# Optimization experiments

Measured on AMD Instinct MI355X. Metric: run time of the kernel, lower is better.

## Reference

```python
import jax, jax.numpy as jnp
import numpy as np

B, S, Z = 64, 512, 256
HID, L = 1024, 1024


def _lstm_cell(x, h, c, Wih, Whh, bih, bhh):
    # torch LSTMCell gate order: i, f, g, o
    gates = x @ Wih.T + bih + h @ Whh.T + bhh  # [B, 4L]
    i, f, g, o = jnp.split(gates, 4, axis=-1)
    i, f, o = jax.nn.sigmoid(i), jax.nn.sigmoid(f), jax.nn.sigmoid(o)
    g = jnp.tanh(g)
    c_new = f * c + i * g
    h_new = o * jnp.tanh(c_new)
    return h_new, c_new


def setup_inputs() -> dict:
    key = jax.random.key(0)
    ks = jax.random.split(key, 16)
    sc = 0.05
    return {
        "z": jax.random.normal(ks[0], (B, S, Z), jnp.float32),
        "prev_gen0": jax.random.uniform(ks[1], (B, Z), jnp.float32),
        "h1": jnp.zeros((B, L), jnp.float32),
        "c1": jnp.zeros((B, L), jnp.float32),
        "h2": jnp.zeros((B, L), jnp.float32),
        "c2": jnp.zeros((B, L), jnp.float32),
        "W1": jax.random.normal(ks[2], (HID, 2 * Z), jnp.float32) * sc,
        "b1": jnp.zeros((HID,), jnp.float32),
        "Wih1": jax.random.normal(ks[3], (4 * L, HID), jnp.float32) * sc,
        "Whh1": jax.random.normal(ks[4], (4 * L, L), jnp.float32) * sc,
        "bih1": jnp.zeros((4 * L,), jnp.float32),
        "bhh1": jnp.zeros((4 * L,), jnp.float32),
        "Wih2": jax.random.normal(ks[5], (4 * L, L), jnp.float32) * sc,
        "Whh2": jax.random.normal(ks[6], (4 * L, L), jnp.float32) * sc,
        "bih2": jnp.zeros((4 * L,), jnp.float32),
        "bhh2": jnp.zeros((4 * L,), jnp.float32),
        "W2": jax.random.normal(ks[7], (Z, L), jnp.float32) * sc,
        "b2": jnp.zeros((Z,), jnp.float32),
    }


def reference(z, prev_gen0, h1, c1, h2, c2, W1, b1, Wih1, Whh1, bih1, bhh1,
              Wih2, Whh2, bih2, bhh2, W2, b2):
    z_t = jnp.transpose(z, (1, 0, 2))  # [S, B, Z]

    def step(carry, z_step):
        prev_gen, h1, c1, h2, c2 = carry
        concat_in = jnp.concatenate([z_step, prev_gen], axis=-1)  # [B, 2Z]
        out = jax.nn.relu(concat_in @ W1.T + b1)                  # [B, HID]
        h1, c1 = _lstm_cell(out, h1, c1, Wih1, Whh1, bih1, bhh1)
        # dropout disabled (inference / deterministic reference)
        h2, c2 = _lstm_cell(h1, h2, c2, Wih2, Whh2, bih2, bhh2)
        prev_gen = h2 @ W2.T + b2                                 # [B, Z]
        return (prev_gen, h1, c1, h2, c2), prev_gen

    (_, h1, c1, h2, c2), feats = jax.lax.scan(
        step, (prev_gen0, h1, c1, h2, c2), z_t)
    gen_feats = jnp.transpose(feats, (1, 0, 2))  # [B, S, Z]
    return gen_feats, (h1, c1), (h2, c2)
```

## Files before the change

### kernel.cpp

```cpp
#include <hip/hip_runtime.h>

#define NB 64
#define NS 512
#define NZ 256
#define NH 1024
#define NWG 256
#define NT 512

typedef _Float16 f16;
typedef unsigned long long u64;
typedef __attribute__((ext_vector_type(8))) _Float16 half8;
typedef __attribute__((ext_vector_type(4))) float f32x4;

#define WS_BAR  0
#define WS_B1P  32768
#define WS_PG0  36864
#define WS_WF   69632
#define WS_ACT  2166784
#define SLOTF 65536
#define REQ1 (2166784ull + 3ull * 513ull * 131072ull)

__device__ __forceinline__ float sigf(float x) { return 1.f / (1.f + __expf(-x)); }
__device__ __forceinline__ float tanhfast(float x) { return 2.f / (1.f + __expf(-2.f * x)) - 1.f; }

__device__ __forceinline__ f32x4 MF(half8 a, half8 b, f32x4 c) {
  return __builtin_amdgcn_mfma_f32_16x16x32_f16(a, b, c, 0, 0, 0);
}

__device__ __forceinline__ u64 ald8(const f16* p) {
  return __hip_atomic_load((const u64*)p, __ATOMIC_RELAXED, __HIP_MEMORY_SCOPE_AGENT);
}
template <bool CACHED>
__device__ __forceinline__ half8 ldc(const f16* base, int kk, int kg, int R) {
  int ch = 8 * kk + 2 * kg;
  union { u64 u[2]; half8 h; } x;
  if (CACHED) {
    x.u[0] = *(const u64*)(base + ((size_t)(ch * 64 + R) * 4));
    x.u[1] = *(const u64*)(base + ((size_t)((ch + 1) * 64 + R) * 4));
  } else {
    x.u[0] = ald8(base + ((size_t)(ch * 64 + R) * 4));
    x.u[1] = ald8(base + ((size_t)((ch + 1) * 64 + R) * 4));
  }
  return x.h;
}
__device__ __forceinline__ void ast4f(float* p, float v) {
  __hip_atomic_store((unsigned*)(void*)p, __float_as_uint(v), __ATOMIC_RELAXED, __HIP_MEMORY_SCOPE_AGENT);
}
__device__ __forceinline__ void store_act(f16* base, int w, int m, float hvf) {
  f16 hv = (f16)hvf;
  unsigned short hb; __builtin_memcpy(&hb, &hv, 2);
  int l = threadIdx.x & 63;
  int c_ = l & 15;
  int v1 = __shfl((int)hb, c_ + 16);
  int v2 = __shfl((int)hb, c_ + 32);
  int v3 = __shfl((int)hb, c_ + 48);
  if (l < 16) {
    int R = 16 * m + c_;
    u64 val = (u64)hb | ((u64)(unsigned short)v1 << 16)
            | ((u64)(unsigned short)v2 << 32) | ((u64)(unsigned short)v3 << 48);
    __hip_atomic_store((u64*)(base + ((size_t)(w * 64 + R) * 4)), val,
                       __ATOMIC_RELAXED, __HIP_MEMORY_SCOPE_AGENT);
  }
}
template <bool CACHED>
__device__ __forceinline__ void gemm_half(const f16* base, const char* brow, int bofs,
                                          int kh, int kg, int R, f32x4& a0, f32x4& a1) {
  #pragma unroll 8
  for (int i = 0; i < 16; ++i) {
    int kk = kh * 16 + i;
    half8 a = ldc<CACHED>(base, kk, kg, R);
    half8 b = *(const half8*)(brow + bofs + kk * 64);
    if (i & 1) a1 = MF(a, b, a1); else a0 = MF(a, b, a0);
  }
}

__device__ __forceinline__ void bar_arrive(char* bar, int w, unsigned e) {
  asm volatile("s_waitcnt vmcnt(0)" ::: "memory");
  __syncthreads();
  if (threadIdx.x == 0)
    __hip_atomic_store((unsigned*)(bar + (size_t)w * 128), e,
                       __ATOMIC_RELAXED, __HIP_MEMORY_SCOPE_AGENT);
}
__device__ __forceinline__ void bar_wait(char* bar, unsigned e) {
  if (threadIdx.x < 64) {
    const unsigned* c0 = (const unsigned*)(bar + (size_t)threadIdx.x * 128);
    for (;;) {
      unsigned v0 = __hip_atomic_load(c0,            __ATOMIC_RELAXED, __HIP_MEMORY_SCOPE_AGENT);
      unsigned v1 = __hip_atomic_load(c0 + 64 * 32,  __ATOMIC_RELAXED, __HIP_MEMORY_SCOPE_AGENT);
      unsigned v2 = __hip_atomic_load(c0 + 128 * 32, __ATOMIC_RELAXED, __HIP_MEMORY_SCOPE_AGENT);
      unsigned v3 = __hip_atomic_load(c0 + 192 * 32, __ATOMIC_RELAXED, __HIP_MEMORY_SCOPE_AGENT);
      int ok = (v0 >= e) & (v1 >= e) & (v2 >= e) & (v3 >= e);
      if (__all(ok)) break;
      __builtin_amdgcn_s_sleep(1);
    }
    asm volatile("" ::: "memory");
  }
  __syncthreads();
}

#define L_W0   0
#define L_W2   10304
#define L_W1   12368
#define L_WP2  78160
#define L_W1P  143952
#define L_X    146064
#define L_X2   150160
#define L_X3   154256
#define LDS_BYTES 154512

__global__ void init_state(const float* __restrict__ h1, const float* __restrict__ h2,
                           const float* __restrict__ pg0, const float* __restrict__ W1,
                           const float* __restrict__ b1, const float* __restrict__ b2,
                           char* __restrict__ ws, size_t h2off) {
  int i = blockIdx.x * blockDim.x + threadIdx.x;
  int R = i & 63;
  int U = i >> 6;
  f16* H1s0 = (f16*)(ws + WS_ACT);
  f16* H2s0 = (f16*)(ws + WS_ACT) + h2off;
  int pidx = ((U >> 2) * 64 + R) * 4 + (U & 3);
  H1s0[pidx] = (f16)h1[(size_t)R * NH + U];
  H2s0[pidx] = (f16)h2[(size_t)R * NH + U];
  if (i < 16384) {
    int u = i >> 6, r2 = i & 63;
    ((f16*)(ws + WS_PG0))[((u >> 2) * 64 + r2) * 4 + (u & 3)] = (f16)pg0[(size_t)r2 * NZ + u];
  }
  if (i < NH) {
    float acc = b1[i];
    const float* wp = W1 + (size_t)i * (2 * NZ) + NZ;
    for (int mm = 0; mm < NZ; ++mm) acc = fmaf(wp[mm], b2[mm], acc);
    ((float*)(ws + WS_B1P))[i] = acc;
  }
  if (i < 8192) ((unsigned*)(ws + WS_BAR))[i] = 0u;
}

__global__ void prep_wfused(const float* __restrict__ W1, const float* __restrict__ W2,
                            char* __restrict__ ws) {
  int u = blockIdx.x >> 2;
  int j = ((blockIdx.x & 3) << 8) + threadIdx.x;
  const float* wp = W1 + (size_t)u * (2 * NZ) + NZ;
  float acc = 0.f;
  for (int mm = 0; mm < NZ; ++mm) acc = fmaf(wp[mm], W2[(size_t)mm * NH + j], acc);
  ((f16*)(ws + WS_WF))[(size_t)u * NH + j] = (f16)acc;
}

template <bool CACHED>
__global__ __launch_bounds__(NT, 1) void gen_persistent(
    const float* __restrict__ z,
    const float* __restrict__ W1, const float* __restrict__ b1,
    const float* __restrict__ Wih1, const float* __restrict__ Whh1,
    const float* __restrict__ bih1, const float* __restrict__ bhh1,
    const float* __restrict__ Wih2, const float* __restrict__ Whh2,
    const float* __restrict__ bih2, const float* __restrict__ bhh2,
    const float* __restrict__ W2, const float* __restrict__ b2,
    const float* __restrict__ c1in, const float* __restrict__ c2in,
    float* __restrict__ dout, char* __restrict__ ws, size_t h2off, size_t outoff)
{
  extern __shared__ char smem[];
  const int w = blockIdx.x;
  const int tid = threadIdx.x;
  const int w8 = tid >> 6;
  const int m = w8 & 3;
  const int kh = w8 >> 2;
  const int l = tid & 63;
  const int c = l & 15;
  const int kg = l >> 4;

  f16* H1base = (f16*)(ws + WS_ACT);
  f16* H2base = H1base + h2off;
  f16* Outbase = H1base + outoff;
  const f16* Pg0p = (const f16*)(ws + WS_PG0);
  const f16* Wf = (const f16*)(ws + WS_WF);
  const float* b1p = (const float*)(ws + WS_B1P);
  char* bar = ws + WS_BAR;

  for (int i = 0; i < 16; ++i) {
    int gi = i >> 2, uu = 4 * w + (i & 3);
    const float* s1i = Wih1 + (size_t)(gi * NH + uu) * NH;
    const float* s1h = Whh1 + (size_t)(gi * NH + uu) * NH;
    const float* s2i = Wih2 + (size_t)(gi * NH + uu) * NH;
    const float* s2h = Whh2 + (size_t)(gi * NH + uu) * NH;
    f16* d1 = (f16*)(smem + L_W1 + i * 4112);
    f16* d2 = (f16*)(smem + L_WP2 + i * 4112);
    for (int k = tid; k < NH; k += NT) {
      d1[k] = (f16)s1i[k]; d1[NH + k] = (f16)s1h[k];
      d2[k] = (f16)s2i[k]; d2[NH + k] = (f16)s2h[k];
    }
  }
  for (int i = 0; i < 4; ++i) {
    int uu = 4 * w + i;
    f16* d0 = (f16*)(smem + L_W0 + i * 2576);
    if (tid < 256) d0[tid] = (f16)W1[(size_t)uu * (2 * NZ) + tid];
    for (int k = tid; k < NH; k += NT) d0[NZ + k] = Wf[(size_t)uu * NH + k];
    f16* dp = (f16*)(smem + L_W1P + i * 528);
    if (tid < 256) dp[tid] = (f16)W1[(size_t)uu * (2 * NZ) + NZ + tid];
  }
  {
    f16* dw2 = (f16*)(smem + L_W2);
    for (int k = tid; k < NH; k += NT) dw2[k] = (f16)W2[(size_t)w * NH + k];
  }
  __syncthreads();

  const int R = 16 * m + c;
  const int U = 4 * w + kg;
  const float b0fused = b1p[U];
  const float b0plain = b1[U];
  const float bi1 = bih1[U] + bhh1[U];
  const float bf1 = bih1[NH + U] + bhh1[NH + U];
  const float bg1 = bih1[2 * NH + U] + bhh1[2 * NH + U];
  const float bo1 = bih1[3 * NH + U] + bhh1[3 * NH + U];
  const float bi2 = bih2[U] + bhh2[U];
  const float bf2 = bih2[NH + U] + bhh2[NH + U];
  const float bg2 = bih2[2 * NH + U] + bhh2[2 * NH + U];
  const float bo2 = bih2[3 * NH + U] + bhh2[3 * NH + U];
  const float b2w = b2[w];

  float c1reg = c1in[(size_t)R * NH + U];
  float c2reg = c2in[(size_t)R * NH + U];
  float h1last = 0.f, h2last = 0.f;

  float* scr  = (float*)(smem + L_X) + m * 256;
  float* scr3 = (float*)(smem + L_X3) + m * 16;
  const char* brow0 = smem + L_W0 + (c & 3) * 2576 + kg * 16;
  const char* brow2 = smem + L_W2 + kg * 16;
  const char* brow1 = smem + L_W1 + c * 4112 + kg * 16;
  const char* browp2 = smem + L_WP2 + c * 4112 + kg * 16;
  const char* browp0 = smem + L_W1P + (c & 3) * 528 + kg * 16;
  const float* zlane = z + (size_t)R * NS * NZ + kg * 8;

  for (int t = 0; t < NS; ++t) {
    const int sp = CACHED ? t : (t & 1);
    const int sn = CACHED ? (t + 1) : ((t + 1) & 1);
    const f16* h2prev = H2base + (size_t)sp * SLOTF;
    const f16* h1prev = H1base + (size_t)sp * SLOTF;
    f16* h1new = H1base + (size_t)sn * SLOTF;
    f16* h2new = H2base + (size_t)sn * SLOTF;
    f16* outb = Outbase + (size_t)sn * SLOTF;
    const unsigned eb = 3u * (unsigned)t;

    f32x4 ao0 = {0.f,0.f,0.f,0.f}, ao1 = ao0, ap0 = ao0, ap1 = ao0;
    if (t == 0) {
      if (kh == 0) {
        #pragma unroll
        for (int kk = 0; kk < 8; ++kk) {
          f32x4 f0 = *(const f32x4*)(zlane + kk * 32);
          f32x4 f1 = *(const f32x4*)(zlane + kk * 32 + 4);
          half8 a;
          a[0]=(f16)f0[0]; a[1]=(f16)f0[1]; a[2]=(f16)f0[2]; a[3]=(f16)f0[3];
          a[4]=(f16)f1[0]; a[5]=(f16)f1[1]; a[6]=(f16)f1[2]; a[7]=(f16)f1[3];
          half8 b = *(const half8*)(brow0 + kk * 64);
          if (kk & 1) ao1 = MF(a, b, ao1); else ao0 = MF(a, b, ao0);
        }
      } else {
        #pragma unroll
        for (int kk = 0; kk < 8; ++kk) {
          half8 a = ldc<true>(Pg0p, kk, kg, R);
          half8 b = *(const half8*)(browp0 + kk * 64);
          if (kk & 1) ao1 = MF(a, b, ao1); else ao0 = MF(a, b, ao0);
        }
      }
      bar_wait(bar, eb);
    } else {
      const float* zt = zlane + (size_t)t * NZ;
      #pragma unroll
      for (int i = 0; i < 4; ++i) {
        int kk = kh * 4 + i;
        f32x4 f0 = *(const f32x4*)(zt + kk * 32);
        f32x4 f1 = *(const f32x4*)(zt + kk * 32 + 4);
        half8 a;
        a[0]=(f16)f0[0]; a[1]=(f16)f0[1]; a[2]=(f16)f0[2]; a[3]=(f16)f0[3];
        a[4]=(f16)f1[0]; a[5]=(f16)f1[1]; a[6]=(f16)f1[2]; a[7]=(f16)f1[3];
        half8 b = *(const half8*)(brow0 + kk * 64);
        if (i & 1) ao1 = MF(a, b, ao1); else ao0 = MF(a, b, ao0);
      }
      bar_wait(bar, eb);
      #pragma unroll 8
      for (int i = 0; i < 16; ++i) {
        int kk = kh * 16 + i;
        half8 a = ldc<CACHED>(h2prev, kk, kg, R);
        half8 bwf = *(const half8*)(brow0 + 512 + kk * 64);
        half8 bw2 = *(const half8*)(brow2 + kk * 64);
        if (i & 1) { ao1 = MF(a, bwf, ao1); ap1 = MF(a, bw2, ap1); }
        else       { ao0 = MF(a, bwf, ao0); ap0 = MF(a, bw2, ap0); }
      }
    }
    f32x4 Dp;
    {
      float* s2 = (float*)(smem + L_X2) + m * 256;
      f32x4 D = ao0 + ao1;
      Dp = ap0 + ap1;
      if (kh == 0) {
        if (c < 4) {
          #pragma unroll
          for (int v = 0; v < 4; ++v) s2[c * 16 + kg * 4 + v] = D[v];
        }
        if (c == 0 && t > 0) {
          #pragma unroll
          for (int v = 0; v < 4; ++v) scr3[kg * 4 + v] = Dp[v];
        }
      }
      __syncthreads();
      if (kh == 1) {
        if (c < 4) {
          #pragma unroll
          for (int v = 0; v < 4; ++v) scr[c * 16 + kg * 4 + v] = D[v] + s2[c * 16 + kg * 4 + v];
        }
        float pre = scr[kg * 16 + c] + ((t == 0) ? b0plain : b0fused);
        store_act(outb, w, m, fmaxf(pre, 0.f));
      }
    }
    bar_arrive(bar, w, eb + 1);
    if (kh == 1 && t > 0 && c == 0) {
      #pragma unroll
      for (int v = 0; v < 4; ++v) {
        int Rp = 16 * m + kg * 4 + v;
        ast4f(&dout[((size_t)Rp * NS + (t - 1)) * NZ + w], Dp[v] + scr3[kg * 4 + v] + b2w);
      }
    }

    {
      f32x4 g0 = {0.f,0.f,0.f,0.f}, g1 = g0;
      gemm_half<CACHED>(h1prev, brow1, 2048, kh, kg, R, g0, g1);
      bar_wait(bar, eb + 1);
      gemm_half<CACHED>(outb, brow1, 0, kh, kg, R, g0, g1);
      float* s2 = (float*)(smem + L_X2) + m * 256;
      f32x4 D = g0 + g1;
      if (kh == 0) {
        #pragma unroll
        for (int v = 0; v < 4; ++v) s2[c * 16 + kg * 4 + v] = D[v];
      }
      __syncthreads();
      if (kh == 1) {
        #pragma unroll
        for (int v = 0; v < 4; ++v) scr[c * 16 + kg * 4 + v] = D[v] + s2[c * 16 + kg * 4 + v];
        float ai = scr[kg * 16 + c];
        float af = scr[(4 + kg) * 16 + c];
        float ag = scr[(8 + kg) * 16 + c];
        float aoo = scr[(12 + kg) * 16 + c];
        float iv = sigf(ai + bi1), fv = sigf(af + bf1);
        float gv = tanhfast(ag + bg1), ov = sigf(aoo + bo1);
        float cn = fmaf(fv, c1reg, iv * gv);
        c1reg = cn;
        float hv = ov * tanhfast(cn);
        h1last = hv;
        store_act(h1new, w, m, hv);
      }
    }
    bar_arrive(bar, w, eb + 2);

    {
      f32x4 q0 = {0.f,0.f,0.f,0.f}, q1 = q0;
      gemm_half<CACHED>(h2prev, browp2, 2048, kh, kg, R, q0, q1);
      bar_wait(bar, eb + 2);
      gemm_half<CACHED>(h1new, browp2, 0, kh, kg, R, q0, q1);
      float* s2 = (float*)(smem + L_X2) + m * 256;
      f32x4 D = q0 + q1;
      if (kh == 0) {
        #pragma unroll
        for (int v = 0; v < 4; ++v) s2[c * 16 + kg * 4 + v] = D[v];
      }
      __syncthreads();
      if (kh == 1) {
        #pragma unroll
        for (int v = 0; v < 4; ++v) scr[c * 16 + kg * 4 + v] = D[v] + s2[c * 16 + kg * 4 + v];
        float ai = scr[kg * 16 + c];
        float af = scr[(4 + kg) * 16 + c];
        float ag = scr[(8 + kg) * 16 + c];
        float aoo = scr[(12 + kg) * 16 + c];
        float iv = sigf(ai + bi2), fv = sigf(af + bf2);
        float gv = tanhfast(ag + bg2), ov = sigf(aoo + bo2);
        float cn = fmaf(fv, c2reg, iv * gv);
        c2reg = cn;
        float hv = ov * tanhfast(cn);
        h2last = hv;
        store_act(h2new, w, m, hv);
      }
    }
    bar_arrive(bar, w, eb + 3);
  }

  bar_wait(bar, 3u * NS);
  {
    const f16* h2fin = H2base + (size_t)(CACHED ? NS : 0) * SLOTF;
    f32x4 t0 = {0.f,0.f,0.f,0.f}, t1 = t0;
    gemm_half<CACHED>(h2fin, brow2, 0, kh, kg, R, t0, t1);
    f32x4 Dp2 = t0 + t1;
    if (kh == 0 && c == 0) {
      #pragma unroll
      for (int v = 0; v < 4; ++v) scr3[kg * 4 + v] = Dp2[v];
    }
    __syncthreads();
    if (kh == 1 && c == 0) {
      #pragma unroll
      for (int v = 0; v < 4; ++v) {
        int Rp = 16 * m + kg * 4 + v;
        dout[((size_t)Rp * NS + (NS - 1)) * NZ + w] = Dp2[v] + scr3[kg * 4 + v] + b2w;
      }
    }
  }

  if (kh == 1) {
    float* o = dout + (size_t)NB * NS * NZ;
    o[(size_t)R * NH + U] = h1last;
    o[(size_t)NB * NH + (size_t)R * NH + U] = c1reg;
    o[2 * (size_t)NB * NH + (size_t)R * NH + U] = h2last;
    o[3 * (size_t)NB * NH + (size_t)R * NH + U] = c2reg;
  }
}

extern "C" void kernel_launch(void* const* d_in, const int* in_sizes, int n_in,
                              void* d_out, int out_size, void* d_ws, size_t ws_size,
                              hipStream_t stream) {
  const float* z    = (const float*)d_in[0];
  const float* pg0  = (const float*)d_in[1];
  const float* h1   = (const float*)d_in[2];
  const float* c1   = (const float*)d_in[3];
  const float* h2   = (const float*)d_in[4];
  const float* c2   = (const float*)d_in[5];
  const float* W1   = (const float*)d_in[6];
  const float* b1   = (const float*)d_in[7];
  const float* Wih1 = (const float*)d_in[8];
  const float* Whh1 = (const float*)d_in[9];
  const float* bih1 = (const float*)d_in[10];
  const float* bhh1 = (const float*)d_in[11];
  const float* Wih2 = (const float*)d_in[12];
  const float* Whh2 = (const float*)d_in[13];
  const float* bih2 = (const float*)d_in[14];
  const float* bhh2 = (const float*)d_in[15];
  const float* W2   = (const float*)d_in[16];
  const float* b2   = (const float*)d_in[17];
  char* ws = (char*)d_ws;
  float* out = (float*)d_out;

  const bool big = ws_size >= (size_t)REQ1;
  const size_t h2off  = big ? (size_t)513 * SLOTF : (size_t)2 * SLOTF;
  const size_t outoff = big ? (size_t)1026 * SLOTF : (size_t)4 * SLOTF;

  hipLaunchKernelGGL(init_state, dim3(256), dim3(256), 0, stream,
                     h1, h2, pg0, W1, b1, b2, ws, h2off);
  hipLaunchKernelGGL(prep_wfused, dim3(4096), dim3(256), 0, stream, W1, W2, ws);
  if (big) {
    hipLaunchKernelGGL((gen_persistent<true>), dim3(NWG), dim3(NT), LDS_BYTES, stream,
                       z, W1, b1, Wih1, Whh1, bih1, bhh1, Wih2, Whh2, bih2, bhh2, W2, b2,
                       c1, c2, out, ws, h2off, outoff);
  } else {
    hipLaunchKernelGGL((gen_persistent<false>), dim3(NWG), dim3(NT), LDS_BYTES, stream,
                       z, W1, b1, Wih1, Whh1, bih1, bhh1, Wih2, Whh2, bih2, bhh2, W2, b2,
                       c1, c2, out, ws, h2off, outoff);
  }
}
```

Before: 9.068 ms.

## Drop split-K warp pairs and replace block barriers with per-wave LDS epoch sync

Halves the threads per workgroup so each wave computes a full K reduction instead of splitting K across two wave groups, which removes the LDS partial-sum exchange and the __syncthreads between halves. The cross-workgroup barrier becomes wave-granular: wave 0 polls global flags and publishes an epoch in LDS that the other waves spin on, and arrivals are counted with an LDS atomic so the last of the four waves signals globally. This cuts intra-block synchronisation on the per-step critical path. In exchange each wave does twice the serial MFMA and load work per step, and there is less parallelism to hide latency.

```diff
diff --git a/kernel.cpp b/kernel.cpp
--- a/kernel.cpp
+++ b/kernel.cpp
@@ -5,7 +5,7 @@
 #define NZ 256
 #define NH 1024
 #define NWG 256
-#define NT 512
+#define NT 256
 
 typedef _Float16 f16;
 typedef unsigned long long u64;
@@ -63,27 +63,19 @@
   }
 }
 template <bool CACHED>
-__device__ __forceinline__ void gemm_half(const f16* base, const char* brow, int bofs,
-                                          int kh, int kg, int R, f32x4& a0, f32x4& a1) {
+__device__ __forceinline__ void gemm_full(const f16* base, const char* brow, int bofs,
+                                          int kg, int R, f32x4& a0, f32x4& a1) {
   #pragma unroll 8
-  for (int i = 0; i < 16; ++i) {
-    int kk = kh * 16 + i;
+  for (int kk = 0; kk < 32; ++kk) {
     half8 a = ldc<CACHED>(base, kk, kg, R);
     half8 b = *(const half8*)(brow + bofs + kk * 64);
-    if (i & 1) a1 = MF(a, b, a1); else a0 = MF(a, b, a0);
-  }
-}
-
-__device__ __forceinline__ void bar_arrive(char* bar, int w, unsigned e) {
-  asm volatile("s_waitcnt vmcnt(0)" ::: "memory");
-  __syncthreads();
-  if (threadIdx.x == 0)
-    __hip_atomic_store((unsigned*)(bar + (size_t)w * 128), e,
-                       __ATOMIC_RELAXED, __HIP_MEMORY_SCOPE_AGENT);
-}
-__device__ __forceinline__ void bar_wait(char* bar, unsigned e) {
-  if (threadIdx.x < 64) {
-    const unsigned* c0 = (const unsigned*)(bar + (size_t)threadIdx.x * 128);
+    if (kk & 1) a1 = MF(a, b, a1); else a0 = MF(a, b, a0);
+  }
+}
+
+__device__ __forceinline__ void bar_wait(char* bar, unsigned* eph, unsigned e, int w4) {
+  if (w4 == 0) {
+    const unsigned* c0 = (const unsigned*)(bar + (size_t)(threadIdx.x & 63) * 128);
     for (;;) {
       unsigned v0 = __hip_atomic_load(c0,            __ATOMIC_RELAXED, __HIP_MEMORY_SCOPE_AGENT);
       unsigned v1 = __hip_atomic_load(c0 + 64 * 32,  __ATOMIC_RELAXED, __HIP_MEMORY_SCOPE_AGENT);
@@ -93,9 +85,22 @@
       if (__all(ok)) break;
       __builtin_amdgcn_s_sleep(1);
     }
-    asm volatile("" ::: "memory");
-  }
-  __syncthreads();
+    if ((threadIdx.x & 63) == 0)
+      __hip_atomic_store(eph, e, __ATOMIC_RELEASE, __HIP_MEMORY_SCOPE_WORKGROUP);
+  } else {
+    while (__hip_atomic_load(eph, __ATOMIC_ACQUIRE, __HIP_MEMORY_SCOPE_WORKGROUP) < e)
+      __builtin_amdgcn_s_sleep(1);
+  }
+  asm volatile("" ::: "memory");
+}
+__device__ __forceinline__ void bar_arrive(char* bar, int w, unsigned* cnt) {
+  asm volatile("s_waitcnt vmcnt(0)" ::: "memory");
+  if ((threadIdx.x & 63) == 0) {
+    unsigned prev = __hip_atomic_fetch_add(cnt, 1u, __ATOMIC_ACQ_REL, __HIP_MEMORY_SCOPE_WORKGROUP);
+    if (((prev + 1u) & 3u) == 0u)
+      __hip_atomic_store((unsigned*)(bar + (size_t)w * 128), (prev + 1u) >> 2,
+                         __ATOMIC_RELAXED, __HIP_MEMORY_SCOPE_AGENT);
+  }
 }
 
 #define L_W0   0
@@ -104,9 +109,8 @@
 #define L_WP2  78160
 #define L_W1P  143952
 #define L_X    146064
-#define L_X2   150160
-#define L_X3   154256
-#define LDS_BYTES 154512
+#define L_CTR  150160
+#define LDS_BYTES 150176
 
 __global__ void init_state(const float* __restrict__ h1, const float* __restrict__ h2,
                            const float* __restrict__ pg0, const float* __restrict__ W1,
@@ -158,9 +162,7 @@
   extern __shared__ char smem[];
   const int w = blockIdx.x;
   const int tid = threadIdx.x;
-  const int w8 = tid >> 6;
-  const int m = w8 & 3;
-  const int kh = w8 >> 2;
+  const int m = tid >> 6;
   const int l = tid & 63;
   const int c = l & 15;
   const int kg = l >> 4;
@@ -172,6 +174,8 @@
   const f16* Wf = (const f16*)(ws + WS_WF);
   const float* b1p = (const float*)(ws + WS_B1P);
   char* bar = ws + WS_BAR;
+  unsigned* EPOCH = (unsigned*)(smem + L_CTR);
+  unsigned* ARRCNT = EPOCH + 1;
 
   for (int i = 0; i < 16; ++i) {
     int gi = i >> 2, uu = 4 * w + (i & 3);
@@ -189,15 +193,16 @@
   for (int i = 0; i < 4; ++i) {
     int uu = 4 * w + i;
     f16* d0 = (f16*)(smem + L_W0 + i * 2576);
-    if (tid < 256) d0[tid] = (f16)W1[(size_t)uu * (2 * NZ) + tid];
+    d0[tid] = (f16)W1[(size_t)uu * (2 * NZ) + tid];
     for (int k = tid; k < NH; k += NT) d0[NZ + k] = Wf[(size_t)uu * NH + k];
     f16* dp = (f16*)(smem + L_W1P + i * 528);
-    if (tid < 256) dp[tid] = (f16)W1[(size_t)uu * (2 * NZ) + NZ + tid];
+    dp[tid] = (f16)W1[(size_t)uu * (2 * NZ) + NZ + tid];
   }
   {
     f16* dw2 = (f16*)(smem + L_W2);
     for (int k = tid; k < NH; k += NT) dw2[k] = (f16)W2[(size_t)w * NH + k];
   }
+  if (tid == 0) { *EPOCH = 0u; *ARRCNT = 0u; }
   __syncthreads();
 
   const int R = 16 * m + c;
@@ -218,8 +223,7 @@
   float c2reg = c2in[(size_t)R * NH + U];
   float h1last = 0.f, h2last = 0.f;
 
-  float* scr  = (float*)(smem + L_X) + m * 256;
-  float* scr3 = (float*)(smem + L_X3) + m * 16;
+  float* scr = (float*)(smem + L_X) + m * 256;
   const char* brow0 = smem + L_W0 + (c & 3) * 2576 + kg * 16;
   const char* brow2 = smem + L_W2 + kg * 16;
   const char* brow1 = smem + L_W1 + c * 4112 + kg * 16;
@@ -238,167 +242,119 @@
     const unsigned eb = 3u * (unsigned)t;
 
     f32x4 ao0 = {0.f,0.f,0.f,0.f}, ao1 = ao0, ap0 = ao0, ap1 = ao0;
-    if (t == 0) {
-      if (kh == 0) {
-        #pragma unroll
-        for (int kk = 0; kk < 8; ++kk) {
-          f32x4 f0 = *(const f32x4*)(zlane + kk * 32);
-          f32x4 f1 = *(const f32x4*)(zlane + kk * 32 + 4);
-          half8 a;
-          a[0]=(f16)f0[0]; a[1]=(f16)f0[1]; a[2]=(f16)f0[2]; a[3]=(f16)f0[3];
-          a[4]=(f16)f1[0]; a[5]=(f16)f1[1]; a[6]=(f16)f1[2]; a[7]=(f16)f1[3];
-          half8 b = *(const half8*)(brow0 + kk * 64);
-          if (kk & 1) ao1 = MF(a, b, ao1); else ao0 = MF(a, b, ao0);
-        }
-      } else {
+    {
+      const float* zt = zlane + (size_t)t * NZ;
+      #pragma unroll
+      for (int kk = 0; kk < 8; ++kk) {
+        f32x4 f0 = *(const f32x4*)(zt + kk * 32);
+        f32x4 f1 = *(const f32x4*)(zt + kk * 32 + 4);
+        half8 a;
+        a[0]=(f16)f0[0]; a[1]=(f16)f0[1]; a[2]=(f16)f0[2]; a[3]=(f16)f0[3];
+        a[4]=(f16)f1[0]; a[5]=(f16)f1[1]; a[6]=(f16)f1[2]; a[7]=(f16)f1[3];
+        half8 b = *(const half8*)(brow0 + kk * 64);
+        if (kk & 1) ao1 = MF(a, b, ao1); else ao0 = MF(a, b, ao0);
+      }
+      if (t == 0) {
         #pragma unroll
         for (int kk = 0; kk < 8; ++kk) {
           half8 a = ldc<true>(Pg0p, kk, kg, R);
           half8 b = *(const half8*)(browp0 + kk * 64);
           if (kk & 1) ao1 = MF(a, b, ao1); else ao0 = MF(a, b, ao0);
         }
-      }
-      bar_wait(bar, eb);
-    } else {
-      const float* zt = zlane + (size_t)t * NZ;
-      #pragma unroll
-      for (int i = 0; i < 4; ++i) {
-        int kk = kh * 4 + i;
-        f32x4 f0 = *(const f32x4*)(zt + kk * 32);
-        f32x4 f1 = *(const f32x4*)(zt + kk * 32 + 4);
-        half8 a;
-        a[0]=(f16)f0[0]; a[1]=(f16)f0[1]; a[2]=(f16)f0[2]; a[3]=(f16)f0[3];
-        a[4]=(f16)f1[0]; a[5]=(f16)f1[1]; a[6]=(f16)f1[2]; a[7]=(f16)f1[3];
-        half8 b = *(const half8*)(brow0 + kk * 64);
-        if (i & 1) ao1 = MF(a, b, ao1); else ao0 = MF(a, b, ao0);
-      }
-      bar_wait(bar, eb);
-      #pragma unroll 8
-      for (int i = 0; i < 16; ++i) {
-        int kk = kh * 16 + i;
-        half8 a = ldc<CACHED>(h2prev, kk, kg, R);
-        half8 bwf = *(const half8*)(brow0 + 512 + kk * 64);
-        half8 bw2 = *(const half8*)(brow2 + kk * 64);
-        if (i & 1) { ao1 = MF(a, bwf, ao1); ap1 = MF(a, bw2, ap1); }
-        else       { ao0 = MF(a, bwf, ao0); ap0 = MF(a, bw2, ap0); }
+        bar_wait(bar, EPOCH, eb, m);
+      } else {
+        bar_wait(bar, EPOCH, eb, m);
+        #pragma unroll 8
+        for (int kk = 0; kk < 32; ++kk) {
+          half8 a = ldc<CACHED>(h2prev, kk, kg, R);
+          half8 bwf = *(const half8*)(brow0 + 512 + kk * 64);
+          half8 bw2 = *(const half8*)(brow2 + kk * 64);
+          if (kk & 1) { ao1 = MF(a, bwf, ao1); ap1 = MF(a, bw2, ap1); }
+          else        { ao0 = MF(a, bwf, ao0); ap0 = MF(a, bw2, ap0); }
+        }
       }
     }
     f32x4 Dp;
     {
-      float* s2 = (float*)(smem + L_X2) + m * 256;
       f32x4 D = ao0 + ao1;
       Dp = ap0 + ap1;
-      if (kh == 0) {
-        if (c < 4) {
-          #pragma unroll
-          for (int v = 0; v < 4; ++v) s2[c * 16 + kg * 4 + v] = D[v];
-        }
-        if (c == 0 && t > 0) {
-          #pragma unroll
-          for (int v = 0; v < 4; ++v) scr3[kg * 4 + v] = Dp[v];
-        }
+      if (c < 4) {
+        #pragma unroll
+        for (int v = 0; v < 4; ++v) scr[c * 16 + kg * 4 + v] = D[v];
       }
-      __syncthreads();
-      if (kh == 1) {
-        if (c < 4) {
-          #pragma unroll
-          for (int v = 0; v < 4; ++v) scr[c * 16 + kg * 4 + v] = D[v] + s2[c * 16 + kg * 4 + v];
-        }
-        float pre = scr[kg * 16 + c] + ((t == 0) ? b0plain : b0fused);
-        store_act(outb, w, m, fmaxf(pre, 0.f));
-      }
-    }
-    bar_arrive(bar, w, eb + 1);
-    if (kh == 1 && t > 0 && c == 0) {
+      float pre = scr[kg * 16 + c] + ((t == 0) ? b0plain : b0fused);
+      store_act(outb, w, m, fmaxf(pre, 0.f));
+    }
+    bar_arrive(bar, w, ARRCNT);
+    if (t > 0 && c == 0) {
       #pragma unroll
       for (int v = 0; v < 4; ++v) {
         int Rp = 16 * m + kg * 4 + v;
-        ast4f(&dout[((size_t)Rp * NS + (t - 1)) * NZ + w], Dp[v] + scr3[kg * 4 + v] + b2w);
+        ast4f(&dout[((size_t)Rp * NS + (t - 1)) * NZ + w], Dp[v] + b2w);
       }
     }
 
     {
       f32x4 g0 = {0.f,0.f,0.f,0.f}, g1 = g0;
-      gemm_half<CACHED>(h1prev, brow1, 2048, kh, kg, R, g0, g1);
-      bar_wait(bar, eb + 1);
-      gemm_half<CACHED>(outb, brow1, 0, kh, kg, R, g0, g1);
-      float* s2 = (float*)(smem + L_X2) + m * 256;
+      gemm_full<CACHED>(h1prev, brow1, 2048, kg, R, g0, g1);
+      bar_wait(bar, EPOCH, eb + 1, m);
+      gemm_full<CACHED>(outb, brow1, 0, kg, R, g0, g1);
       f32x4 D = g0 + g1;
-      if (kh == 0) {
-        #pragma unroll
-        for (int v = 0; v < 4; ++v) s2[c * 16 + kg * 4 + v] = D[v];
-      }
-      __syncthreads();
-      if (kh == 1) {
-        #pragma unroll
-        for (int v = 0; v < 4; ++v) scr[c * 16 + kg * 4 + v] = D[v] + s2[c * 16 + kg * 4 + v];
-        float ai = scr[kg * 16 + c];
-        float af = scr[(4 + kg) * 16 + c];
-        float ag = scr[(8 + kg) * 16 + c];
-        float aoo = scr[(12 + kg) * 16 + c];
-        float iv = sigf(ai + bi1), fv = sigf(af + bf1);
-        float gv = tanhfast(ag + bg1), ov = sigf(aoo + bo1);
-        float cn = fmaf(fv, c1reg, iv * gv);
-        c1reg = cn;
-        float hv = ov * tanhfast(cn);
-        h1last = hv;
-        store_act(h1new, w, m, hv);
-      }
-    }
-    bar_arrive(bar, w, eb + 2);
+      #pragma unroll
+      for (int v = 0; v < 4; ++v) scr[c * 16 + kg * 4 + v] = D[v];
+      float ai = scr[kg * 16 + c];
+      float af = scr[(4 + kg) * 16 + c];
+      float ag = scr[(8 + kg) * 16 + c];
+      float aoo = scr[(12 + kg) * 16 + c];
+      float iv = sigf(ai + bi1), fv = sigf(af + bf1);
+      float gv = tanhfast(ag + bg1), ov = sigf(aoo + bo1);
+      float cn = fmaf(fv, c1reg, iv * gv);
+      c1reg = cn;
+      float hv = ov * tanhfast(cn);
+      h1last = hv;
+      store_act(h1new, w, m, hv);
+    }
+    bar_arrive(bar, w, ARRCNT);
 
     {
       f32x4 q0 = {0.f,0.f,0.f,0.f}, q1 = q0;
-      gemm_half<CACHED>(h2prev, browp2, 2048, kh, kg, R, q0, q1);
-      bar_wait(bar, eb + 2);
-      gemm_half<CACHED>(h1new, browp2, 0, kh, kg, R, q0, q1);
-      float* s2 = (float*)(smem + L_X2) + m * 256;
+      gemm_full<CACHED>(h2prev, browp2, 2048, kg, R, q0, q1);
+      bar_wait(bar, EPOCH, eb + 2, m);
+      gemm_full<CACHED>(h1new, browp2, 0, kg, R, q0, q1);
       f32x4 D = q0 + q1;
-      if (kh == 0) {
-        #pragma unroll
-        for (int v = 0; v < 4; ++v) s2[c * 16 + kg * 4 + v] = D[v];
-      }
-      __syncthreads();
-      if (kh == 1) {
-        #pragma unroll
-        for (int v = 0; v < 4; ++v) scr[c * 16 + kg * 4 + v] = D[v] + s2[c * 16 + kg * 4 + v];
-        float ai = scr[kg * 16 + c];
-        float af = scr[(4 + kg) * 16 + c];
-        float ag = scr[(8 + kg) * 16 + c];
-        float aoo = scr[(12 + kg) * 16 + c];
-        float iv = sigf(ai + bi2), fv = sigf(af + bf2);
-        float gv = tanhfast(ag + bg2), ov = sigf(aoo + bo2);
-        float cn = fmaf(fv, c2reg, iv * gv);
-        c2reg = cn;
-        float hv = ov * tanhfast(cn);
-        h2last = hv;
-        store_act(h2new, w, m, hv);
-      }
-    }
-    bar_arrive(bar, w, eb + 3);
-  }
-
-  bar_wait(bar, 3u * NS);
+      #pragma unroll
+      for (int v = 0; v < 4; ++v) scr[c * 16 + kg * 4 + v] = D[v];
+      float ai = scr[kg * 16 + c];
+      float af = scr[(4 + kg) * 16 + c];
+      float ag = scr[(8 + kg) * 16 + c];
+      float aoo = scr[(12 + kg) * 16 + c];
+      float iv = sigf(ai + bi2), fv = sigf(af + bf2);
+      float gv = tanhfast(ag + bg2), ov = sigf(aoo + bo2);
+      float cn = fmaf(fv, c2reg, iv * gv);
+      c2reg = cn;
+      float hv = ov * tanhfast(cn);
+      h2last = hv;
+      store_act(h2new, w, m, hv);
+    }
+    bar_arrive(bar, w, ARRCNT);
+  }
+
+  bar_wait(bar, EPOCH, 3u * NS, m);
   {
     const f16* h2fin = H2base + (size_t)(CACHED ? NS : 0) * SLOTF;
     f32x4 t0 = {0.f,0.f,0.f,0.f}, t1 = t0;
-    gemm_half<CACHED>(h2fin, brow2, 0, kh, kg, R, t0, t1);
+    gemm_full<CACHED>(h2fin, brow2, 0, kg, R, t0, t1);
     f32x4 Dp2 = t0 + t1;
-    if (kh == 0 && c == 0) {
-      #pragma unroll
-      for (int v = 0; v < 4; ++v) scr3[kg * 4 + v] = Dp2[v];
-    }
-    __syncthreads();
-    if (kh == 1 && c == 0) {
+    if (c == 0) {
       #pragma unroll
       for (int v = 0; v < 4; ++v) {
         int Rp = 16 * m + kg * 4 + v;
-        dout[((size_t)Rp * NS + (NS - 1)) * NZ + w] = Dp2[v] + scr3[kg * 4 + v] + b2w;
+        dout[((size_t)Rp * NS + (NS - 1)) * NZ + w] = Dp2[v] + b2w;
       }
     }
   }
 
-  if (kh == 1) {
+  {
     float* o = dout + (size_t)NB * NS * NZ;
     o[(size_t)R * NH + U] = h1last;
     o[(size_t)NB * NH + (size_t)R * NH + U] = c1reg;
```

Measured after the change: 18.95 ms. 109% more time.
